# Kernel optimization log

Hardware: AMD Instinct MI355X
Metric: run time of the kernel (lower is better)

Reference implementation:

```python
import jax, jax.numpy as jnp
import numpy as np

EMB = 1024
HEADS = 16
DEPTH = EMB // HEADS
B, S = 8, 1024


def setup_inputs() -> dict:
    key = jax.random.key(0)
    ks = jax.random.split(key, 12)
    sc = 0.02
    return {
        "q": jax.random.normal(ks[0], (B, S, EMB), jnp.float32),
        "k": jax.random.normal(ks[1], (B, S, EMB), jnp.float32),
        "v": jax.random.normal(ks[2], (B, S, EMB), jnp.float32),
        # per-head Dense weights stacked: [H, EMB, DEPTH], biases [H, DEPTH]
        "Wq": jax.random.normal(ks[3], (HEADS, EMB, DEPTH), jnp.float32) * sc,
        "bq": jnp.zeros((HEADS, DEPTH), jnp.float32),
        "Wk": jax.random.normal(ks[4], (HEADS, EMB, DEPTH), jnp.float32) * sc,
        "bk": jnp.zeros((HEADS, DEPTH), jnp.float32),
        "Wv": jax.random.normal(ks[5], (HEADS, EMB, DEPTH), jnp.float32) * sc,
        "bv": jnp.zeros((HEADS, DEPTH), jnp.float32),
        # output Dense: [EMB, EMB], bias [EMB]
        "Wo": jax.random.normal(ks[6], (EMB, EMB), jnp.float32) * sc,
        "bo": jnp.zeros((EMB,), jnp.float32),
    }


def reference(q, k, v, Wq, bq, Wk, bk, Wv, bv, Wo, bo):
    # Per-head Dense projections, batched over heads via einsum.
    # qh: [B, H, S, DEPTH]
    qh = jnp.einsum("bsd,hde->bhse", q, Wq) + bq[None, :, None, :]
    kh = jnp.einsum("bsd,hde->bhse", k, Wk) + bk[None, :, None, :]
    vh = jnp.einsum("bsd,hde->bhse", v, Wv) + bv[None, :, None, :]
    # Scaled dot-product attention per head: logits [B, H, Sq, Sk]
    scale = 1.0 / jnp.sqrt(jnp.asarray(DEPTH, jnp.float32))
    logits = jnp.einsum("bhqe,bhke->bhqk", qh, kh) * scale
    attn = jax.nn.softmax(logits, axis=-1)
    ctx = jnp.einsum("bhqk,bhke->bhqe", attn, vh)  # [B, H, S, DEPTH]
    # concat heads along last axis (head order preserved)
    ctx = jnp.transpose(ctx, (0, 2, 1, 3)).reshape(B, S, EMB)
    return ctx @ Wo + bo
```

## Files before the change

kernel.cpp:

```cpp
#include <hip/hip_runtime.h>
#include <hip/hip_bf16.h>
#include <stdint.h>

typedef __bf16 bf16;
typedef __attribute__((ext_vector_type(8))) __bf16 bf16x8;
typedef __attribute__((ext_vector_type(4))) __bf16 bf16x4;
typedef __attribute__((ext_vector_type(4))) float f32x4;

#define GLD(g, l) __builtin_amdgcn_global_load_lds( \
    (const __attribute__((address_space(1))) void*)(g), \
    (__attribute__((address_space(3))) void*)(l), 16, 0, 0)

__device__ __forceinline__ f32x4 mfma16(bf16x8 a, bf16x8 b, f32x4 c) {
  return __builtin_amdgcn_mfma_f32_16x16x32_bf16(a, b, c, 0, 0, 0);
}
__device__ __forceinline__ float fexp2(float x) {
  return __builtin_amdgcn_exp2f(x);
}
__device__ __forceinline__ bf16x8 cvt8(const float4& a, const float4& b) {
  bf16x8 p;
  p[0] = (bf16)a.x; p[1] = (bf16)a.y; p[2] = (bf16)a.z; p[3] = (bf16)a.w;
  p[4] = (bf16)b.x; p[5] = (bf16)b.y; p[6] = (bf16)b.z; p[7] = (bf16)b.w;
  return p;
}

__device__ __forceinline__ void compute128(const bf16* buf, int wr, int wc,
                                           int lr, int quad,
                                           f32x4 (&acc)[4][4]) {
  bf16x8 af[4], bfr[4];
#pragma unroll
  for (int i = 0; i < 4; i++) {
    const int ra = wr + i * 16 + lr;
    const int rb = wc + i * 16 + lr;
    af[i]  = *(const bf16x8*)(buf + ra * 32 + ((quad ^ ((ra >> 1) & 3)) * 8));
    bfr[i] = *(const bf16x8*)(buf + 4096 + rb * 32 +
                              ((quad ^ ((rb >> 1) & 3)) * 8));
  }
  __builtin_amdgcn_s_setprio(1);
#pragma unroll
  for (int im = 0; im < 4; im++)
#pragma unroll
    for (int in = 0; in < 4; in++)
      acc[im][in] = mfma16(af[im], bfr[in], acc[im][in]);
  __builtin_amdgcn_s_setprio(0);
}

#define WAIT_BAR(cnt)                                            \
  asm volatile("s_waitcnt vmcnt(" #cnt ")" ::: "memory");        \
  __builtin_amdgcn_s_barrier();                                  \
  asm volatile("" ::: "memory")

__global__ void wtransA(const float* __restrict__ Wq, const float* __restrict__ Wk,
                        const float* __restrict__ Wv, const float* __restrict__ Wo,
                        bf16* __restrict__ WT, bf16* __restrict__ WoT,
                        const float* __restrict__ q, const float* __restrict__ k,
                        bf16* __restrict__ qc, bf16* __restrict__ kc)
{
  __shared__ bf16 t[32][33];
  const int w = blockIdx.z;
  const int tx = threadIdx.x, ty = threadIdx.y;
  if (w < 3) {
    const float* W = (w == 0) ? Wq : (w == 1) ? Wk : Wv;
    const int h = blockIdx.x >> 1;
    const int c0 = (blockIdx.x & 1) * 32;
    const int r0 = blockIdx.y * 32;
    const float* s = W + (size_t)h * 65536;
    bf16* d = WT + (size_t)w * (1 << 20) + (size_t)h * 65536;
#pragma unroll
    for (int i = 0; i < 32; i += 8)
      t[ty + i][tx] = (bf16)s[(r0 + ty + i) * 64 + c0 + tx];
    __syncthreads();
#pragma unroll
    for (int i = 0; i < 32; i += 8)
      d[(c0 + ty + i) * 1024 + r0 + tx] = t[tx][ty + i];
  } else if (w == 3) {
    const int c0 = blockIdx.x * 32, r0 = blockIdx.y * 32;
#pragma unroll
    for (int i = 0; i < 32; i += 8)
      t[ty + i][tx] = (bf16)Wo[(r0 + ty + i) * 1024 + c0 + tx];
    __syncthreads();
#pragma unroll
    for (int i = 0; i < 32; i += 8)
      WoT[(c0 + ty + i) * 1024 + r0 + tx] = t[tx][ty + i];
  } else {
    const int tid = ty * 32 + tx;
    const int lb = (w - 4) * 1024 + blockIdx.y * 32 + blockIdx.x;
    const float* s = (lb < 4096) ? q : k;
    bf16* d = (lb < 4096) ? qc : kc;
    const size_t base = ((size_t)(lb & 4095) * 256 + tid) * 8;
    float4 a = *(const float4*)(s + base);
    float4 b = *(const float4*)(s + base + 4);
    *(bf16x8*)(d + base) = cvt8(a, b);
  }
}

__global__ __launch_bounds__(256) void proj_qkv(
    const bf16* __restrict__ qc, const bf16* __restrict__ kc,
    const float* __restrict__ v, const bf16* __restrict__ WT,
    const float* __restrict__ bq, const float* __restrict__ bk,
    const float* __restrict__ bv, bf16* __restrict__ qh,
    bf16* __restrict__ kh, bf16* __restrict__ vt, float cscale)
{
  __shared__ bf16 S[24576];
  const int tid = threadIdx.x;
  const int wave = tid >> 6, lane = tid & 63;
  const int lr = lane & 15, quad = lane >> 4;
  const int n0 = blockIdx.x * 128;
  const int mt = blockIdx.y;
  const int mseg = mt * 128;
  const int seg = mseg >> 13;
  const int m0 = mseg & 8191;
  const int wr = (wave >> 1) * 64, wc = (wave & 1) * 64;

  const float* bias = (seg == 0) ? bq : (seg == 1) ? bk : bv;
  const bf16* Bt = WT + (size_t)seg * (1 << 20);

  f32x4 acc[4][4];
#pragma unroll
  for (int i = 0; i < 4; i++)
#pragma unroll
    for (int j = 0; j < 4; j++)
#pragma unroll
      for (int e = 0; e < 4; e++) acc[i][j][e] = 0.f;

  const int srow = tid >> 2;
  const int sko = ((tid & 3) ^ ((srow >> 1) & 3)) * 8;
  const bf16* bPtr = Bt + (size_t)(n0 + srow) * 1024 + sko;

  int i0 = 0, i1 = 1, i2 = 2;

  if (seg < 2) {
    const bf16* Ab = (seg == 1) ? kc : qc;
    const bf16* aPtr = Ab + (size_t)(m0 + srow) * 1024 + sko;
#pragma unroll
    for (int t = 0; t < 2; ++t) {
      bf16* nb = S + t * 8192;
      GLD(aPtr + t * 32,             nb + tid * 8);
      GLD(aPtr + 64 * 1024 + t * 32, nb + 2048 + tid * 8);
      GLD(bPtr + t * 32,             nb + 4096 + tid * 8);
      GLD(bPtr + 64 * 1024 + t * 32, nb + 6144 + tid * 8);
    }
    for (int it = 0; it < 30; ++it) {
      WAIT_BAR(4);
      const int k0 = (it + 2) * 32;
      bf16* nb = S + i2 * 8192;
      GLD(aPtr + k0,             nb + tid * 8);
      GLD(aPtr + 64 * 1024 + k0, nb + 2048 + tid * 8);
      GLD(bPtr + k0,             nb + 4096 + tid * 8);
      GLD(bPtr + 64 * 1024 + k0, nb + 6144 + tid * 8);
      compute128(S + i0 * 8192, wr, wc, lr, quad, acc);
      const int t = i0; i0 = i1; i1 = i2; i2 = t;
    }
    WAIT_BAR(4);
    compute128(S + i0 * 8192, wr, wc, lr, quad, acc);
    WAIT_BAR(0);
    compute128(S + i1 * 8192, wr, wc, lr, quad, acc);
  } else {
    const int ar = tid >> 1, acb = (tid & 1) * 2;
    const int asw = (ar >> 1) & 3;
    const float* vPtr = v + (size_t)(m0 + ar) * 1024 + acb * 8;
    float4 f[4];
#pragma unroll
    for (int j = 0; j < 4; j++) f[j] = *(const float4*)(vPtr + j * 4);
    {
      *(bf16x8*)(S + ar * 32 + ((acb ^ asw) * 8))       = cvt8(f[0], f[1]);
      *(bf16x8*)(S + ar * 32 + (((acb + 1) ^ asw) * 8)) = cvt8(f[2], f[3]);
    }
    GLD(bPtr,                  S + 4096 + tid * 8);
    GLD(bPtr + 64 * 1024,      S + 6144 + tid * 8);
    GLD(bPtr + 32,             S + 8192 + 4096 + tid * 8);
    GLD(bPtr + 64 * 1024 + 32, S + 8192 + 6144 + tid * 8);
    asm volatile("s_waitcnt vmcnt(2)" ::: "memory");
    for (int it = 0; it < 32; ++it) {
      asm volatile("s_waitcnt lgkmcnt(0)" ::: "memory");
      __builtin_amdgcn_sched_barrier(0);
      __builtin_amdgcn_s_barrier();
      asm volatile("" ::: "memory");
      const bool moreA = (it + 1 < 32);
      if (moreA) {
        const int k0 = (it + 1) * 32;
#pragma unroll
        for (int j = 0; j < 4; j++) f[j] = *(const float4*)(vPtr + k0 + j * 4);
      }
      if (it + 2 < 32) {
        const int k0 = (it + 2) * 32;
        bf16* nb = S + i2 * 8192;
        GLD(bPtr + k0,             nb + 4096 + tid * 8);
        GLD(bPtr + 64 * 1024 + k0, nb + 6144 + tid * 8);
      }
      compute128(S + i0 * 8192, wr, wc, lr, quad, acc);
      if (moreA) {
        bf16* nb = S + i1 * 8192;
        *(bf16x8*)(nb + ar * 32 + ((acb ^ asw) * 8))       = cvt8(f[0], f[1]);
        *(bf16x8*)(nb + ar * 32 + (((acb + 1) ^ asw) * 8)) = cvt8(f[2], f[3]);
      }
      const int t = i0; i0 = i1; i1 = i2; i2 = t;
    }
  }

  const int qd = quad * 4;
  float bv4[4];
#pragma unroll
  for (int in = 0; in < 4; in++) bv4[in] = bias[n0 + wc + in * 16 + lr];

  if (seg < 2) {
    bf16* C = (seg == 0) ? qh : kh;
    const float cmul = (seg == 0) ? cscale : 1.0f;
#pragma unroll
    for (int im = 0; im < 4; im++) {
      const int row = m0 + wr + im * 16 + qd;
#pragma unroll
      for (int in = 0; in < 4; in++) {
        const int col = n0 + wc + in * 16 + lr;
#pragma unroll
        for (int i = 0; i < 4; i++)
          C[(size_t)(row + i) * 1024 + col] = (bf16)((acc[im][in][i] + bv4[in]) * cmul);
      }
    }
  } else {
#pragma unroll
    for (int im = 0; im < 4; im++) {
      const int row = m0 + wr + im * 16 + qd;
      const int b = row >> 10, sin = row & 1023;
#pragma unroll
      for (int in = 0; in < 4; in++) {
        const int col = n0 + wc + in * 16 + lr;
        const int h = col >> 6, e = col & 63;
        bf16x4 pk;
#pragma unroll
        for (int i = 0; i < 4; i++) pk[i] = (bf16)(acc[im][in][i] + bv4[in]);
        *(bf16x4*)(vt + (size_t)(b * 16 + h) * 65536 + e * 1024 + sin) = pk;
      }
    }
  }
}

__global__ __launch_bounds__(256) void gemm_a16_c32(
    const bf16* __restrict__ A, const bf16* __restrict__ Bt,
    const float* __restrict__ bias, float* __restrict__ C)
{
  __shared__ bf16 S[24576];
  const int tid = threadIdx.x;
  const int wave = tid >> 6, lane = tid & 63;
  const int lr = lane & 15, quad = lane >> 4;
  const int n0 = blockIdx.x * 128;
  const int m0 = blockIdx.y * 128;
  const int wr = (wave >> 1) * 64, wc = (wave & 1) * 64;

  f32x4 acc[4][4];
#pragma unroll
  for (int i = 0; i < 4; i++)
#pragma unroll
    for (int j = 0; j < 4; j++)
#pragma unroll
      for (int e = 0; e < 4; e++) acc[i][j][e] = 0.f;

  const int srow = tid >> 2;
  const int sko = ((tid & 3) ^ ((srow >> 1) & 3)) * 8;
  const bf16* aPtr = A + (size_t)(m0 + srow) * 1024 + sko;
  const bf16* bPtr = Bt + (size_t)(n0 + srow) * 1024 + sko;

  int i0 = 0, i1 = 1, i2 = 2;
#pragma unroll
  for (int t = 0; t < 2; ++t) {
    bf16* nb = S + t * 8192;
    GLD(aPtr + t * 32,             nb + tid * 8);
    GLD(aPtr + 64 * 1024 + t * 32, nb + 2048 + tid * 8);
    GLD(bPtr + t * 32,             nb + 4096 + tid * 8);
    GLD(bPtr + 64 * 1024 + t * 32, nb + 6144 + tid * 8);
  }
  for (int it = 0; it < 30; ++it) {
    WAIT_BAR(4);
    const int k0 = (it + 2) * 32;
    bf16* nb = S + i2 * 8192;
    GLD(aPtr + k0,             nb + tid * 8);
    GLD(aPtr + 64 * 1024 + k0, nb + 2048 + tid * 8);
    GLD(bPtr + k0,             nb + 4096 + tid * 8);
    GLD(bPtr + 64 * 1024 + k0, nb + 6144 + tid * 8);
    compute128(S + i0 * 8192, wr, wc, lr, quad, acc);
    const int t = i0; i0 = i1; i1 = i2; i2 = t;
  }
  WAIT_BAR(4);
  compute128(S + i0 * 8192, wr, wc, lr, quad, acc);
  WAIT_BAR(0);
  compute128(S + i1 * 8192, wr, wc, lr, quad, acc);

  const int qd = quad * 4;
  float bv4[4];
#pragma unroll
  for (int in = 0; in < 4; in++) bv4[in] = bias[n0 + wc + in * 16 + lr];
#pragma unroll
  for (int im = 0; im < 4; im++) {
    const int row = m0 + wr + im * 16 + qd;
#pragma unroll
    for (int in = 0; in < 4; in++) {
      const int col = n0 + wc + in * 16 + lr;
#pragma unroll
      for (int i = 0; i < 4; i++)
        C[(size_t)(row + i) * 1024 + col] = acc[im][in][i] + bv4[in];
    }
  }
}

__global__ __launch_bounds__(256) void attn_k(
    const bf16* Q, const bf16* __restrict__ Kh,
    const bf16* __restrict__ Vt, bf16* O)
{
  __shared__ bf16 sK[64 * 72];
  __shared__ bf16 sV[64 * 72];
  __shared__ bf16 sP[128 * 72];
  const int q0 = blockIdx.x * 128, h = blockIdx.y, b = blockIdx.z;
  const int tid = threadIdx.x, wave = tid >> 6, lane = tid & 63;
  const int lr = lane & 15, quad = lane >> 4, kq = quad * 8;
  const int wq = wave * 32;

  const bf16* Qb = Q + (size_t)(b * 1024 + q0) * 1024 + h * 64;
  const bf16* Kb = Kh + (size_t)(b * 1024) * 1024 + h * 64;
  const bf16* Vb = Vt + (size_t)(b * 16 + h) * 65536;

  bf16x8 qf[2][2];
#pragma unroll
  for (int rg = 0; rg < 2; rg++)
#pragma unroll
    for (int ks = 0; ks < 2; ks++)
      qf[rg][ks] = *(const bf16x8*)(Qb + (wq + rg * 16 + lr) * 1024 + ks * 32 + kq);

  f32x4 o[2][4];
  float rsum[2][4];
#pragma unroll
  for (int rg = 0; rg < 2; rg++) {
#pragma unroll
    for (int et = 0; et < 4; et++)
#pragma unroll
      for (int e = 0; e < 4; e++) o[rg][et][e] = 0.f;
#pragma unroll
    for (int i = 0; i < 4; i++) rsum[rg][i] = 0.f;
  }

  const int r = tid >> 3;
  const int c = (tid & 7) * 8;

  bf16x8 k1 = *(const bf16x8*)(Kb + (size_t)r * 1024 + c);
  bf16x8 k2 = *(const bf16x8*)(Kb + (size_t)(32 + r) * 1024 + c);
  bf16x8 v1 = *(const bf16x8*)(Vb + (size_t)r * 1024 + c);
  bf16x8 v2 = *(const bf16x8*)(Vb + (size_t)(32 + r) * 1024 + c);

  for (int kv0 = 0; kv0 < 1024; kv0 += 64) {
    __syncthreads();
    *(bf16x8*)(sK + r * 72 + c) = k1;
    *(bf16x8*)(sK + (32 + r) * 72 + c) = k2;
    *(bf16x8*)(sV + r * 72 + c) = v1;
    *(bf16x8*)(sV + (32 + r) * 72 + c) = v2;
    __syncthreads();
    if (kv0 + 64 < 1024) {
      k1 = *(const bf16x8*)(Kb + (size_t)(kv0 + 64 + r) * 1024 + c);
      k2 = *(const bf16x8*)(Kb + (size_t)(kv0 + 96 + r) * 1024 + c);
      v1 = *(const bf16x8*)(Vb + (size_t)r * 1024 + kv0 + 64 + c);
      v2 = *(const bf16x8*)(Vb + (size_t)(32 + r) * 1024 + kv0 + 64 + c);
    }

    f32x4 sc[2][4];
    __builtin_amdgcn_s_setprio(1);
#pragma unroll
    for (int nt = 0; nt < 4; nt++) {
      bf16x8 kf0 = *(const bf16x8*)(sK + (nt * 16 + lr) * 72 + kq);
      bf16x8 kf1 = *(const bf16x8*)(sK + (nt * 16 + lr) * 72 + 32 + kq);
#pragma unroll
      for (int rg = 0; rg < 2; rg++) {
        f32x4 z;
#pragma unroll
        for (int e = 0; e < 4; e++) z[e] = 0.f;
        z = mfma16(qf[rg][0], kf0, z);
        z = mfma16(qf[rg][1], kf1, z);
        sc[rg][nt] = z;
      }
    }
    __builtin_amdgcn_s_setprio(0);

#pragma unroll
    for (int rg = 0; rg < 2; rg++)
#pragma unroll
      for (int i = 0; i < 4; i++) {
        float p0 = fexp2(sc[rg][0][i]);
        float p1 = fexp2(sc[rg][1][i]);
        float p2 = fexp2(sc[rg][2][i]);
        float p3 = fexp2(sc[rg][3][i]);
        rsum[rg][i] += (p0 + p1) + (p2 + p3);
        const int prow = (wq + rg * 16 + quad * 4 + i) * 72;
        sP[prow + 0 * 16 + lr] = (bf16)p0;
        sP[prow + 1 * 16 + lr] = (bf16)p1;
        sP[prow + 2 * 16 + lr] = (bf16)p2;
        sP[prow + 3 * 16 + lr] = (bf16)p3;
      }

    bf16x8 pa[2], pb[2];
#pragma unroll
    for (int rg = 0; rg < 2; rg++) {
      pa[rg] = *(const bf16x8*)(sP + (wq + rg * 16 + lr) * 72 + kq);
      pb[rg] = *(const bf16x8*)(sP + (wq + rg * 16 + lr) * 72 + 32 + kq);
    }
    __builtin_amdgcn_s_setprio(1);
#pragma unroll
    for (int et = 0; et < 4; et++) {
      bf16x8 vf0 = *(const bf16x8*)(sV + (et * 16 + lr) * 72 + kq);
      bf16x8 vf1 = *(const bf16x8*)(sV + (et * 16 + lr) * 72 + 32 + kq);
#pragma unroll
      for (int rg = 0; rg < 2; rg++) {
        o[rg][et] = mfma16(pa[rg], vf0, o[rg][et]);
        o[rg][et] = mfma16(pb[rg], vf1, o[rg][et]);
      }
    }
    __builtin_amdgcn_s_setprio(0);
  }

#pragma unroll
  for (int rg = 0; rg < 2; rg++)
#pragma unroll
    for (int i = 0; i < 4; i++) {
      float rs = rsum[rg][i];
#pragma unroll
      for (int off = 1; off < 16; off <<= 1)
        rs += __shfl_xor(rs, off, 64);
      rsum[rg][i] = 1.f / rs;
    }

  bf16* Ob = O + (size_t)(b * 1024 + q0) * 1024 + h * 64;
#pragma unroll
  for (int rg = 0; rg < 2; rg++)
#pragma unroll
    for (int i = 0; i < 4; i++) {
      const int row = wq + rg * 16 + quad * 4 + i;
#pragma unroll
      for (int et = 0; et < 4; et++)
        Ob[row * 1024 + et * 16 + lr] = (bf16)(o[rg][et][i] * rsum[rg][i]);
    }
}

extern "C" void kernel_launch(void* const* d_in, const int* in_sizes, int n_in,
                              void* d_out, int out_size, void* d_ws, size_t ws_size,
                              hipStream_t stream)
{
  const float* q  = (const float*)d_in[0];
  const float* k  = (const float*)d_in[1];
  const float* v  = (const float*)d_in[2];
  const float* Wq = (const float*)d_in[3];
  const float* bq = (const float*)d_in[4];
  const float* Wk = (const float*)d_in[5];
  const float* bk = (const float*)d_in[6];
  const float* Wv = (const float*)d_in[7];
  const float* bv = (const float*)d_in[8];
  const float* Wo = (const float*)d_in[9];
  const float* bo = (const float*)d_in[10];
  float* out = (float*)d_out;
  bf16* ws = (bf16*)d_ws;

  const int MB = 1 << 20;
  bf16* WT  = ws;
  bf16* qh  = ws + 3 * MB;
  bf16* kh  = ws + 11 * MB;
  bf16* vt  = ws + 19 * MB;
  bf16* WoT = ws + 27 * MB;
  bf16* qc  = (bf16*)d_out;
  bf16* kc  = (bf16*)d_out + 8 * MB;

  const float cscale = 0.1803368801111601f;

  dim3 tb(32, 8);
  wtransA<<<dim3(32, 32, 12), tb, 0, stream>>>(Wq, Wk, Wv, Wo, WT, WoT,
                                               q, k, qc, kc);

  proj_qkv<<<dim3(8, 192), 256, 0, stream>>>(qc, kc, v, WT, bq, bk, bv,
                                             qh, kh, vt, cscale);

  attn_k<<<dim3(8, 16, 8), 256, 0, stream>>>(qh, kh, vt, qh);

  gemm_a16_c32<<<dim3(8, 64), 256, 0, stream>>>(qh, WoT, bo, out);
}
```

Measured before the change: 325.3 us.

## Load GEMM B fragments directly into registers, bypassing LDS staging

In both the QKV projection and the output GEMM, the weight (B) operand is no longer staged through shared memory. Each wave now reads its B MFMA fragments straight from global memory into registers, one K-step ahead, and only the A tile stays triple-buffered in LDS. The goal is to halve the LDS footprint and LDS read traffic, which could raise occupancy. In exchange, waves sharing a column block re-read the same B data, the global reads are strided by row and less coalesced, and the loop relies on compiler-inserted waits for the last A buffer.

Result: slower. 378.3 us (+16.3%).

```diff
diff --git a/kernel.cpp b/kernel.cpp
--- a/kernel.cpp
+++ b/kernel.cpp
@@ -24,31 +24,34 @@
   return p;
 }
 
-__device__ __forceinline__ void compute128(const bf16* buf, int wr, int wc,
-                                           int lr, int quad,
-                                           f32x4 (&acc)[4][4]) {
-  bf16x8 af[4], bfr[4];
-#pragma unroll
-  for (int i = 0; i < 4; i++) {
-    const int ra = wr + i * 16 + lr;
-    const int rb = wc + i * 16 + lr;
-    af[i]  = *(const bf16x8*)(buf + ra * 32 + ((quad ^ ((ra >> 1) & 3)) * 8));
-    bfr[i] = *(const bf16x8*)(buf + 4096 + rb * 32 +
-                              ((quad ^ ((rb >> 1) & 3)) * 8));
-  }
-  __builtin_amdgcn_s_setprio(1);
-#pragma unroll
-  for (int im = 0; im < 4; im++)
-#pragma unroll
-    for (int in = 0; in < 4; in++)
-      acc[im][in] = mfma16(af[im], bfr[in], acc[im][in]);
-  __builtin_amdgcn_s_setprio(0);
-}
-
 #define WAIT_BAR(cnt)                                            \
   asm volatile("s_waitcnt vmcnt(" #cnt ")" ::: "memory");        \
   __builtin_amdgcn_s_barrier();                                  \
   asm volatile("" ::: "memory")
+
+__device__ __forceinline__ void computeA(const bf16* abuf, int wr, int lr,
+                                         int quad, const bf16x8 (&bc)[4],
+                                         f32x4 (&acc)[4][4]) {
+  bf16x8 af[4];
+#pragma unroll
+  for (int i = 0; i < 4; i++) {
+    const int ra = wr + i * 16 + lr;
+    af[i] = *(const bf16x8*)(abuf + ra * 32 + ((quad ^ ((ra >> 1) & 3)) * 8));
+  }
+  __builtin_amdgcn_s_setprio(1);
+#pragma unroll
+  for (int im = 0; im < 4; im++)
+#pragma unroll
+    for (int in = 0; in < 4; in++)
+      acc[im][in] = mfma16(af[im], bc[in], acc[im][in]);
+  __builtin_amdgcn_s_setprio(0);
+}
+
+#define LOAD_BFRAG(dst, Bbase, nwc, k0)                                   \
+  _Pragma("unroll")                                                       \
+  for (int i = 0; i < 4; i++)                                             \
+    dst[i] = *(const bf16x8*)(Bbase + (size_t)((nwc) + i * 16 + lr) * 1024 \
+                              + (k0) + kq);
 
 __global__ void wtransA(const float* __restrict__ Wq, const float* __restrict__ Wk,
                         const float* __restrict__ Wv, const float* __restrict__ Wo,
@@ -101,16 +104,17 @@
     const float* __restrict__ bv, bf16* __restrict__ qh,
     bf16* __restrict__ kh, bf16* __restrict__ vt, float cscale)
 {
-  __shared__ bf16 S[24576];
+  __shared__ bf16 S[12288];
   const int tid = threadIdx.x;
   const int wave = tid >> 6, lane = tid & 63;
-  const int lr = lane & 15, quad = lane >> 4;
+  const int lr = lane & 15, quad = lane >> 4, kq = quad * 8;
   const int n0 = blockIdx.x * 128;
   const int mt = blockIdx.y;
   const int mseg = mt * 128;
   const int seg = mseg >> 13;
   const int m0 = mseg & 8191;
   const int wr = (wave >> 1) * 64, wc = (wave & 1) * 64;
+  const int nwc = n0 + wc;
 
   const float* bias = (seg == 0) ? bq : (seg == 1) ? bk : bv;
   const bf16* Bt = WT + (size_t)seg * (1 << 20);
@@ -125,36 +129,32 @@
 
   const int srow = tid >> 2;
   const int sko = ((tid & 3) ^ ((srow >> 1) & 3)) * 8;
-  const bf16* bPtr = Bt + (size_t)(n0 + srow) * 1024 + sko;
-
+
+  bf16x8 bc[4], bn[4];
   int i0 = 0, i1 = 1, i2 = 2;
 
   if (seg < 2) {
     const bf16* Ab = (seg == 1) ? kc : qc;
     const bf16* aPtr = Ab + (size_t)(m0 + srow) * 1024 + sko;
-#pragma unroll
-    for (int t = 0; t < 2; ++t) {
-      bf16* nb = S + t * 8192;
-      GLD(aPtr + t * 32,             nb + tid * 8);
-      GLD(aPtr + 64 * 1024 + t * 32, nb + 2048 + tid * 8);
-      GLD(bPtr + t * 32,             nb + 4096 + tid * 8);
-      GLD(bPtr + 64 * 1024 + t * 32, nb + 6144 + tid * 8);
-    }
-    for (int it = 0; it < 30; ++it) {
-      WAIT_BAR(4);
-      const int k0 = (it + 2) * 32;
-      bf16* nb = S + i2 * 8192;
-      GLD(aPtr + k0,             nb + tid * 8);
-      GLD(aPtr + 64 * 1024 + k0, nb + 2048 + tid * 8);
-      GLD(bPtr + k0,             nb + 4096 + tid * 8);
-      GLD(bPtr + 64 * 1024 + k0, nb + 6144 + tid * 8);
-      compute128(S + i0 * 8192, wr, wc, lr, quad, acc);
+    GLD(aPtr,                  S + tid * 8);
+    GLD(aPtr + 64 * 1024,      S + 2048 + tid * 8);
+    GLD(aPtr + 32,             S + 4096 + tid * 8);
+    GLD(aPtr + 64 * 1024 + 32, S + 4096 + 2048 + tid * 8);
+    LOAD_BFRAG(bc, Bt, nwc, 0);
+    for (int it = 0; it < 32; ++it) {
+      WAIT_BAR(6);
+      if (it + 2 < 32) {
+        const int k0 = (it + 2) * 32;
+        bf16* nb = S + i2 * 4096;
+        GLD(aPtr + k0,             nb + tid * 8);
+        GLD(aPtr + 64 * 1024 + k0, nb + 2048 + tid * 8);
+      }
+      if (it + 1 < 32) { LOAD_BFRAG(bn, Bt, nwc, (it + 1) * 32); }
+      computeA(S + i0 * 4096, wr, lr, quad, bc, acc);
+#pragma unroll
+      for (int i = 0; i < 4; i++) bc[i] = bn[i];
       const int t = i0; i0 = i1; i1 = i2; i2 = t;
     }
-    WAIT_BAR(4);
-    compute128(S + i0 * 8192, wr, wc, lr, quad, acc);
-    WAIT_BAR(0);
-    compute128(S + i1 * 8192, wr, wc, lr, quad, acc);
   } else {
     const int ar = tid >> 1, acb = (tid & 1) * 2;
     const int asw = (ar >> 1) & 3;
@@ -166,11 +166,7 @@
       *(bf16x8*)(S + ar * 32 + ((acb ^ asw) * 8))       = cvt8(f[0], f[1]);
       *(bf16x8*)(S + ar * 32 + (((acb + 1) ^ asw) * 8)) = cvt8(f[2], f[3]);
     }
-    GLD(bPtr,                  S + 4096 + tid * 8);
-    GLD(bPtr + 64 * 1024,      S + 6144 + tid * 8);
-    GLD(bPtr + 32,             S + 8192 + 4096 + tid * 8);
-    GLD(bPtr + 64 * 1024 + 32, S + 8192 + 6144 + tid * 8);
-    asm volatile("s_waitcnt vmcnt(2)" ::: "memory");
+    LOAD_BFRAG(bc, Bt, nwc, 0);
     for (int it = 0; it < 32; ++it) {
       asm volatile("s_waitcnt lgkmcnt(0)" ::: "memory");
       __builtin_amdgcn_sched_barrier(0);
@@ -181,18 +177,15 @@
         const int k0 = (it + 1) * 32;
 #pragma unroll
         for (int j = 0; j < 4; j++) f[j] = *(const float4*)(vPtr + k0 + j * 4);
-      }
-      if (it + 2 < 32) {
-        const int k0 = (it + 2) * 32;
-        bf16* nb = S + i2 * 8192;
-        GLD(bPtr + k0,             nb + 4096 + tid * 8);
-        GLD(bPtr + 64 * 1024 + k0, nb + 6144 + tid * 8);
-      }
-      compute128(S + i0 * 8192, wr, wc, lr, quad, acc);
+        LOAD_BFRAG(bn, Bt, nwc, k0);
+      }
+      computeA(S + i0 * 4096, wr, lr, quad, bc, acc);
       if (moreA) {
-        bf16* nb = S + i1 * 8192;
+        bf16* nb = S + i1 * 4096;
         *(bf16x8*)(nb + ar * 32 + ((acb ^ asw) * 8))       = cvt8(f[0], f[1]);
         *(bf16x8*)(nb + ar * 32 + (((acb + 1) ^ asw) * 8)) = cvt8(f[2], f[3]);
+#pragma unroll
+        for (int i = 0; i < 4; i++) bc[i] = bn[i];
       }
       const int t = i0; i0 = i1; i1 = i2; i2 = t;
     }
@@ -239,13 +232,14 @@
     const bf16* __restrict__ A, const bf16* __restrict__ Bt,
     const float* __restrict__ bias, float* __restrict__ C)
 {
-  __shared__ bf16 S[24576];
+  __shared__ bf16 S[12288];
   const int tid = threadIdx.x;
   const int wave = tid >> 6, lane = tid & 63;
-  const int lr = lane & 15, quad = lane >> 4;
+  const int lr = lane & 15, quad = lane >> 4, kq = quad * 8;
   const int n0 = blockIdx.x * 128;
   const int m0 = blockIdx.y * 128;
   const int wr = (wave >> 1) * 64, wc = (wave & 1) * 64;
+  const int nwc = n0 + wc;
 
   f32x4 acc[4][4];
 #pragma unroll
@@ -258,32 +252,29 @@
   const int srow = tid >> 2;
   const int sko = ((tid & 3) ^ ((srow >> 1) & 3)) * 8;
   const bf16* aPtr = A + (size_t)(m0 + srow) * 1024 + sko;
-  const bf16* bPtr = Bt + (size_t)(n0 + srow) * 1024 + sko;
-
+
+  bf16x8 bc[4], bn[4];
   int i0 = 0, i1 = 1, i2 = 2;
-#pragma unroll
-  for (int t = 0; t < 2; ++t) {
-    bf16* nb = S + t * 8192;
-    GLD(aPtr + t * 32,             nb + tid * 8);
-    GLD(aPtr + 64 * 1024 + t * 32, nb + 2048 + tid * 8);
-    GLD(bPtr + t * 32,             nb + 4096 + tid * 8);
-    GLD(bPtr + 64 * 1024 + t * 32, nb + 6144 + tid * 8);
-  }
-  for (int it = 0; it < 30; ++it) {
-    WAIT_BAR(4);
-    const int k0 = (it + 2) * 32;
-    bf16* nb = S + i2 * 8192;
-    GLD(aPtr + k0,             nb + tid * 8);
-    GLD(aPtr + 64 * 1024 + k0, nb + 2048 + tid * 8);
-    GLD(bPtr + k0,             nb + 4096 + tid * 8);
-    GLD(bPtr + 64 * 1024 + k0, nb + 6144 + tid * 8);
-    compute128(S + i0 * 8192, wr, wc, lr, quad, acc);
+
+  GLD(aPtr,                  S + tid * 8);
+  GLD(aPtr + 64 * 1024,      S + 2048 + tid * 8);
+  GLD(aPtr + 32,             S + 4096 + tid * 8);
+  GLD(aPtr + 64 * 1024 + 32, S + 4096 + 2048 + tid * 8);
+  LOAD_BFRAG(bc, Bt, nwc, 0);
+  for (int it = 0; it < 32; ++it) {
+    WAIT_BAR(6);
+    if (it + 2 < 32) {
+      const int k0 = (it + 2) * 32;
+      bf16* nb = S + i2 * 4096;
+      GLD(aPtr + k0,             nb + tid * 8);
+      GLD(aPtr + 64 * 1024 + k0, nb + 2048 + tid * 8);
+    }
+    if (it + 1 < 32) { LOAD_BFRAG(bn, Bt, nwc, (it + 1) * 32); }
+    computeA(S + i0 * 4096, wr, lr, quad, bc, acc);
+#pragma unroll
+    for (int i = 0; i < 4; i++) bc[i] = bn[i];
     const int t = i0; i0 = i1; i1 = i2; i2 = t;
   }
-  WAIT_BAR(4);
-  compute128(S + i0 * 8192, wr, wc, lr, quad, acc);
-  WAIT_BAR(0);
-  compute128(S + i1 * 8192, wr, wc, lr, quad, acc);
 
   const int qd = quad * 4;
   float bv4[4];
```
